# Performance work log

Measured on AMD Instinct MI355X. Metric: run time of the kernel, lower is better.

## Reference

```python
import jax, jax.numpy as jnp
import numpy as np

N_NODES = 50000
N_EDGES = 600000
D = 128        # input_dim == hidden_dim
OUT = 2        # output_dim
N_LAYERS = 6


def setup_inputs() -> dict:
    key = jax.random.key(0)
    ks = jax.random.split(key, 6)
    scale = 1.0 / np.sqrt(D)
    x = jax.random.normal(ks[0], (N_NODES, D), jnp.float32)
    edge_index = jax.random.randint(ks[1], (2, N_EDGES), 0, N_NODES)
    Wl = jax.random.normal(ks[2], (N_LAYERS, D, D), jnp.float32) * scale  # neighbor (lin_l) weights
    Wr = jax.random.normal(ks[3], (N_LAYERS, D, D), jnp.float32) * scale  # root (lin_r) weights
    bl = jnp.zeros((N_LAYERS, D), jnp.float32)                            # lin_l bias
    fc_W = jax.random.normal(ks[4], (D, OUT), jnp.float32) * scale
    fc_b = jnp.zeros((OUT,), jnp.float32)
    return {"x": x, "edge_index": edge_index, "Wl": Wl, "Wr": Wr, "bl": bl,
            "fc_W": fc_W, "fc_b": fc_b}


def _sage_conv(h, src, dst, deg_inv, Wl_i, Wr_i, bl_i):
    # mean aggregation over incoming edges: gather -> scatter-add -> normalize
    agg = jax.ops.segment_sum(h[src], dst, num_segments=h.shape[0]) * deg_inv  # [N, D]
    return agg @ Wl_i + h @ Wr_i + bl_i


def reference(x, edge_index, Wl, Wr, bl, fc_W, fc_b):
    src, dst = edge_index[0], edge_index[1]
    deg = jax.ops.segment_sum(jnp.ones(src.shape, x.dtype), dst, num_segments=x.shape[0])
    deg_inv = (1.0 / jnp.maximum(deg, 1.0))[:, None]  # [N, 1]
    h = x
    # ReLU follows every SAGEConv: inner act of each GraphSAGE block + explicit F.relu after each block
    for i in range(N_LAYERS):
        h = _sage_conv(h, src, dst, deg_inv, Wl[i], Wr[i], bl[i])
        h = jax.nn.relu(h)
    return h @ fc_W + fc_b  # [N, OUT]
```

## Files before the change

kernel.cpp:

```cpp
#include <hip/hip_runtime.h>
#include <hip/hip_bf16.h>

#define N_NODES 50000
#define N_EDGES 600000
#define DD 128
#define N_LAYERS 6
#define SCAN_BLOCKS 196
#define N_CHUNKS 3125
#define AGG_BLOCKS 6256

#define XB16_T 1600000
#define ZERO_T 50000
#define PREPW_T 196608
#define PREP_TOTAL (XB16_T + ZERO_T + PREPW_T)

typedef __attribute__((ext_vector_type(8))) short bf16x8;
typedef __attribute__((ext_vector_type(4))) float floatx4;

__device__ __forceinline__ void ldsdma16(const void* g, void* l) {
    __builtin_amdgcn_global_load_lds(
        (const __attribute__((address_space(1))) char*)g,
        (__attribute__((address_space(3))) char*)l, 16, 0, 0);
}

__device__ __forceinline__ unsigned short f2b(float f) {
    unsigned u = __float_as_uint(f);
    unsigned r = (u + 0x7FFFu + ((u >> 16) & 1u)) >> 16;
    return (unsigned short)r;
}


__global__ void prep_all(const float* __restrict__ x, unsigned short* __restrict__ hx,
                         const float* __restrict__ Wl, const float* __restrict__ Wr,
                         unsigned short* __restrict__ WT2,
                         int* __restrict__ deg, int* __restrict__ cursor) {
    int gid = blockIdx.x * blockDim.x + threadIdx.x;
    if (gid < XB16_T) {
        int b = gid * 4;
        float4 v = *(const float4*)(x + b);
        ushort4 o;
        o.x = f2b(v.x); o.y = f2b(v.y); o.z = f2b(v.z); o.w = f2b(v.w);
        *(ushort4*)(hx + b) = o;
    } else if (gid < XB16_T + ZERO_T) {
        int i = gid - XB16_T;
        deg[i] = 0; cursor[i] = 0;
    } else if (gid < PREP_TOTAL) {
        int idx = gid - (XB16_T + ZERO_T);
        int l   = idx >> 15;
        int rem = idx & 32767;
        int n   = rem >> 8;
        int k2  = rem & 255;
        const float* W = (k2 < 128 ? Wl : Wr) + (size_t)l * DD * DD + (size_t)(k2 & 127) * DD + n;
        WT2[idx] = f2b(*W);
    }
}


__global__ void count_deg(const int* __restrict__ dst, int* __restrict__ deg) {
    int e = blockIdx.x * blockDim.x + threadIdx.x;
    if (e < N_EDGES) atomicAdd(&deg[dst[e]], 1);
}

__global__ void block_sums(const int* __restrict__ deg, int* __restrict__ bsum) {
    __shared__ int s[256];
    int tid = threadIdx.x;
    int i = blockIdx.x * 256 + tid;
    int v = (i < N_NODES) ? deg[i] : 0;
    s[tid] = v;
    __syncthreads();
    #pragma unroll
    for (int off = 128; off > 0; off >>= 1) {
        if (tid < off) s[tid] += s[tid + off];
        __syncthreads();
    }
    if (tid == 0) bsum[blockIdx.x] = s[0];
}

__global__ void scan_bsums(int* __restrict__ bsum, int* __restrict__ offsets) {
    __shared__ int s[256];
    int tid = threadIdx.x;
    int v = (tid < SCAN_BLOCKS) ? bsum[tid] : 0;
    s[tid] = v;
    __syncthreads();
    for (int off = 1; off < 256; off <<= 1) {
        int t = (tid >= off) ? s[tid - off] : 0;
        __syncthreads();
        s[tid] += t;
        __syncthreads();
    }
    if (tid < SCAN_BLOCKS) bsum[tid] = s[tid] - v;
    if (tid == 0) offsets[N_NODES] = N_EDGES;
}

__global__ void write_offsets(const int* __restrict__ deg, const int* __restrict__ bsum,
                              int* __restrict__ offsets, float* __restrict__ deg_inv) {
    __shared__ int s[256];
    int tid = threadIdx.x;
    int i = blockIdx.x * 256 + tid;
    int v = (i < N_NODES) ? deg[i] : 0;
    s[tid] = v;
    __syncthreads();
    for (int off = 1; off < 256; off <<= 1) {
        int t = (tid >= off) ? s[tid - off] : 0;
        __syncthreads();
        s[tid] += t;
        __syncthreads();
    }
    if (i < N_NODES) {
        offsets[i] = bsum[blockIdx.x] + s[tid] - v;
        deg_inv[i] = 1.0f / (float)(v > 1 ? v : 1);
    }
}

__global__ void fill_csr(const int* __restrict__ src, const int* __restrict__ dst,
                         const int* __restrict__ offsets, int* __restrict__ cursor,
                         int* __restrict__ csr_src) {
    int e = blockIdx.x * blockDim.x + threadIdx.x;
    if (e < N_EDGES) {
        int d = dst[e];
        int p = atomicAdd(&cursor[d], 1);
        csr_src[offsets[d] + p] = src[e];
    }
}


__global__ void aggregate(const unsigned short* __restrict__ hin, const int* __restrict__ offsets,
                          const int* __restrict__ csr_src, const float* __restrict__ deg_inv,
                          unsigned short* __restrict__ agg) {
    int w    = threadIdx.x >> 6;
    int lane = threadIdx.x & 63;
    int nodeSel = lane >> 5;
    int l32  = lane & 31;
    int grp  = l32 >> 3;
    int p    = l32 & 7;

    int b = blockIdx.x;
    int x = b & 7, s = b >> 3;
    int hc = 16 * (s >> 1) + 2 * x + (s & 1);
    int node = hc * 8 + 2 * w + nodeSel;
    if (node >= N_NODES) return;
    int s0 = offsets[node], e0 = offsets[node + 1];
    float di = deg_inv[node];

    float a[16];
    #pragma unroll
    for (int i = 0; i < 16; ++i) a[i] = 0.f;

    const unsigned short* base = hin;
    int j = s0 + grp;
    for (; j + 4 < e0; j += 8) {
        int src1 = csr_src[j];
        int src2 = csr_src[j + 4];
        const uint4* r1 = (const uint4*)(base + (size_t)src1 * DD + p * 16);
        const uint4* r2 = (const uint4*)(base + (size_t)src2 * DD + p * 16);
        uint4 v1a = r1[0], v1b = r1[1];
        uint4 v2a = r2[0], v2b = r2[1];
        a[0] += __uint_as_float(v1a.x << 16); a[1] += __uint_as_float(v1a.x & 0xFFFF0000u);
        a[2] += __uint_as_float(v1a.y << 16); a[3] += __uint_as_float(v1a.y & 0xFFFF0000u);
        a[4] += __uint_as_float(v1a.z << 16); a[5] += __uint_as_float(v1a.z & 0xFFFF0000u);
        a[6] += __uint_as_float(v1a.w << 16); a[7] += __uint_as_float(v1a.w & 0xFFFF0000u);
        a[8] += __uint_as_float(v1b.x << 16); a[9] += __uint_as_float(v1b.x & 0xFFFF0000u);
        a[10]+= __uint_as_float(v1b.y << 16); a[11]+= __uint_as_float(v1b.y & 0xFFFF0000u);
        a[12]+= __uint_as_float(v1b.z << 16); a[13]+= __uint_as_float(v1b.z & 0xFFFF0000u);
        a[14]+= __uint_as_float(v1b.w << 16); a[15]+= __uint_as_float(v1b.w & 0xFFFF0000u);
        a[0] += __uint_as_float(v2a.x << 16); a[1] += __uint_as_float(v2a.x & 0xFFFF0000u);
        a[2] += __uint_as_float(v2a.y << 16); a[3] += __uint_as_float(v2a.y & 0xFFFF0000u);
        a[4] += __uint_as_float(v2a.z << 16); a[5] += __uint_as_float(v2a.z & 0xFFFF0000u);
        a[6] += __uint_as_float(v2a.w << 16); a[7] += __uint_as_float(v2a.w & 0xFFFF0000u);
        a[8] += __uint_as_float(v2b.x << 16); a[9] += __uint_as_float(v2b.x & 0xFFFF0000u);
        a[10]+= __uint_as_float(v2b.y << 16); a[11]+= __uint_as_float(v2b.y & 0xFFFF0000u);
        a[12]+= __uint_as_float(v2b.z << 16); a[13]+= __uint_as_float(v2b.z & 0xFFFF0000u);
        a[14]+= __uint_as_float(v2b.w << 16); a[15]+= __uint_as_float(v2b.w & 0xFFFF0000u);
    }
    if (j < e0) {
        int src1 = csr_src[j];
        const uint4* r1 = (const uint4*)(base + (size_t)src1 * DD + p * 16);
        uint4 v1a = r1[0], v1b = r1[1];
        a[0] += __uint_as_float(v1a.x << 16); a[1] += __uint_as_float(v1a.x & 0xFFFF0000u);
        a[2] += __uint_as_float(v1a.y << 16); a[3] += __uint_as_float(v1a.y & 0xFFFF0000u);
        a[4] += __uint_as_float(v1a.z << 16); a[5] += __uint_as_float(v1a.z & 0xFFFF0000u);
        a[6] += __uint_as_float(v1a.w << 16); a[7] += __uint_as_float(v1a.w & 0xFFFF0000u);
        a[8] += __uint_as_float(v1b.x << 16); a[9] += __uint_as_float(v1b.x & 0xFFFF0000u);
        a[10]+= __uint_as_float(v1b.y << 16); a[11]+= __uint_as_float(v1b.y & 0xFFFF0000u);
        a[12]+= __uint_as_float(v1b.z << 16); a[13]+= __uint_as_float(v1b.z & 0xFFFF0000u);
        a[14]+= __uint_as_float(v1b.w << 16); a[15]+= __uint_as_float(v1b.w & 0xFFFF0000u);
    }

    #pragma unroll
    for (int i = 0; i < 16; ++i) {
        a[i] += __shfl_xor(a[i], 8, 64);
        a[i] += __shfl_xor(a[i], 16, 64);
    }

    if (grp == 0) {
        uint4 o1, o2;
        o1.x = (unsigned)f2b(a[0] * di) | ((unsigned)f2b(a[1] * di) << 16);
        o1.y = (unsigned)f2b(a[2] * di) | ((unsigned)f2b(a[3] * di) << 16);
        o1.z = (unsigned)f2b(a[4] * di) | ((unsigned)f2b(a[5] * di) << 16);
        o1.w = (unsigned)f2b(a[6] * di) | ((unsigned)f2b(a[7] * di) << 16);
        o2.x = (unsigned)f2b(a[8] * di) | ((unsigned)f2b(a[9] * di) << 16);
        o2.y = (unsigned)f2b(a[10]* di) | ((unsigned)f2b(a[11]* di) << 16);
        o2.z = (unsigned)f2b(a[12]* di) | ((unsigned)f2b(a[13]* di) << 16);
        o2.w = (unsigned)f2b(a[14]* di) | ((unsigned)f2b(a[15]* di) << 16);
        uint4* dst = (uint4*)(agg + (size_t)node * DD + p * 16);
        dst[0] = o1;
        dst[1] = o2;
    }
}


__launch_bounds__(512, 2)
__global__ void gemm_resW(const unsigned short* __restrict__ Agg,
                          const unsigned short* __restrict__ H,
                          const unsigned short* __restrict__ WT2,
                          const float* __restrict__ bias,
                          unsigned short* __restrict__ Cout,
                          const float* __restrict__ fcW,
                          const float* __restrict__ fcb,
                          float* __restrict__ out,
                          int doFC) {
    __shared__ __align__(16) unsigned short sW[128 * 256];
    __shared__ __align__(16) unsigned short sA[8][4096];

    int tid  = threadIdx.x;
    int wid  = tid >> 6, lane = tid & 63;
    int l15  = lane & 15, q = lane >> 4;

    for (int t = tid; t < 4096; t += 512) {
        int col = t >> 5, c = t & 31;
        uint4 v = *(const uint4*)(WT2 + (size_t)col * 256 + c * 8);
        *(uint4*)(sW + ((size_t)col * 32 + (c ^ (col & 7))) * 8) = v;
    }
    __syncthreads();

    float bcol[8];
    #pragma unroll
    for (int j = 0; j < 8; ++j) bcol[j] = bias[j * 16 + l15];

    float2 fcw[8];
    float fb0 = 0.f, fb1 = 0.f;
    if (doFC) {
        #pragma unroll
        for (int j = 0; j < 8; ++j) fcw[j] = *(const float2*)(fcW + (j * 16 + l15) * 2);
        fb0 = fcb[0]; fb1 = fcb[1];
    }

    unsigned short* myA = &sA[wid][0];
    int x = blockIdx.x & 7, bb = blockIdx.x >> 3;

    for (int chunk = x + 8 * (bb * 8 + wid); chunk < N_CHUNKS; chunk += 2048) {
        int row0 = chunk * 16;
        #pragma unroll
        for (int i = 0; i < 4; ++i) {
            int r  = i * 4 + q;
            int cg = l15 ^ (r & 7);
            ldsdma16(Agg + (size_t)(row0 + r) * DD + cg * 8, myA + (size_t)i * 512 + lane * 8);
        }
        #pragma unroll
        for (int i = 0; i < 4; ++i) {
            int r  = i * 4 + q;
            int cg = l15 ^ (r & 7);
            ldsdma16(H + (size_t)(row0 + r) * DD + cg * 8, myA + 2048 + (size_t)i * 512 + lane * 8);
        }
        __builtin_amdgcn_s_waitcnt(0);

        floatx4 acc[8];
        #pragma unroll
        for (int j = 0; j < 8; ++j) acc[j] = (floatx4){0.f, 0.f, 0.f, 0.f};

        #pragma unroll
        for (int s = 0; s < 8; ++s) {
            int cglob = s * 4 + q;
            int reg   = cglob >> 4;
            int cin   = cglob & 15;
            bf16x8 aF = *(const bf16x8*)(myA + (size_t)reg * 2048 +
                                         ((size_t)l15 * 16 + (cin ^ (l15 & 7))) * 8);
            #pragma unroll
            for (int j = 0; j < 8; ++j) {
                int col = j * 16 + l15;
                bf16x8 bF = *(const bf16x8*)(sW + ((size_t)col * 32 + (cglob ^ (col & 7))) * 8);
                acc[j] = __builtin_amdgcn_mfma_f32_16x16x32_bf16(aF, bF, acc[j], 0, 0, 0);
            }
        }

        if (!doFC) {
            #pragma unroll
            for (int r = 0; r < 4; ++r) {
                int row = row0 + q * 4 + r;
                #pragma unroll
                for (int j = 0; j < 8; ++j) {
                    float v = acc[j][r] + bcol[j];
                    Cout[(size_t)row * DD + j * 16 + l15] = f2b(fmaxf(v, 0.f));
                }
            }
        } else {
            #pragma unroll
            for (int r = 0; r < 4; ++r) {
                float p0 = 0.f, p1 = 0.f;
                #pragma unroll
                for (int j = 0; j < 8; ++j) {
                    float v = fmaxf(acc[j][r] + bcol[j], 0.f);
                    p0 += v * fcw[j].x;
                    p1 += v * fcw[j].y;
                }
                p0 += __shfl_xor(p0, 1, 64); p1 += __shfl_xor(p1, 1, 64);
                p0 += __shfl_xor(p0, 2, 64); p1 += __shfl_xor(p1, 2, 64);
                p0 += __shfl_xor(p0, 4, 64); p1 += __shfl_xor(p1, 4, 64);
                p0 += __shfl_xor(p0, 8, 64); p1 += __shfl_xor(p1, 8, 64);
                if (l15 == 0) {
                    int row = row0 + q * 4 + r;
                    out[row * 2]     = p0 + fb0;
                    out[row * 2 + 1] = p1 + fb1;
                }
            }
        }
    }
}


extern "C" void kernel_launch(void* const* d_in, const int* in_sizes, int n_in,
                              void* d_out, int out_size, void* d_ws, size_t ws_size,
                              hipStream_t stream) {
    const float* x    = (const float*)d_in[0];
    const int*   ei   = (const int*)d_in[1];
    const float* Wl   = (const float*)d_in[2];
    const float* Wr   = (const float*)d_in[3];
    const float* bl   = (const float*)d_in[4];
    const float* fcW  = (const float*)d_in[5];
    const float* fcb  = (const float*)d_in[6];
    float* out = (float*)d_out;

    const int* srcIdx = ei;
    const int* dstIdx = ei + N_EDGES;

    char* ws = (char*)d_ws;
    size_t off = 0;
    auto bump = [&](size_t bytes) { char* p = ws + off; off = (off + bytes + 255) & ~(size_t)255; return p; };
    int*   deg     = (int*)  bump(N_NODES * 4);
    int*   cursor  = (int*)  bump(N_NODES * 4);
    int*   offsets = (int*)  bump((N_NODES + 1) * 4);
    int*   bsum    = (int*)  bump(SCAN_BLOCKS * 4);
    float* deg_inv = (float*)bump(N_NODES * 4);
    int*   csr     = (int*)  bump(N_EDGES * 4);
    unsigned short* hx   = (unsigned short*)bump((size_t)N_NODES * DD * 2);
    unsigned short* hb0  = (unsigned short*)bump((size_t)N_NODES * DD * 2);
    unsigned short* hb1  = (unsigned short*)bump((size_t)N_NODES * DD * 2);
    unsigned short* agg  = (unsigned short*)bump((size_t)N_NODES * DD * 2);
    unsigned short* WT2  = (unsigned short*)bump((size_t)N_LAYERS * 128 * 256 * 2);
    (void)ws_size;

    prep_all<<<(PREP_TOTAL + 255) / 256, 256, 0, stream>>>(x, hx, Wl, Wr, WT2, deg, cursor);
    count_deg<<<(N_EDGES + 255) / 256, 256, 0, stream>>>(dstIdx, deg);
    block_sums<<<SCAN_BLOCKS, 256, 0, stream>>>(deg, bsum);
    scan_bsums<<<1, 256, 0, stream>>>(bsum, offsets);
    write_offsets<<<SCAN_BLOCKS, 256, 0, stream>>>(deg, bsum, offsets, deg_inv);
    fill_csr<<<(N_EDGES + 255) / 256, 256, 0, stream>>>(srcIdx, dstIdx, offsets, cursor, csr);

    const unsigned short* hin = hx;
    unsigned short* hbuf[2] = { hb0, hb1 };
    for (int l = 0; l < N_LAYERS; ++l) {
        int last = (l == N_LAYERS - 1);
        aggregate<<<AGG_BLOCKS, 256, 0, stream>>>(hin, offsets, csr, deg_inv, agg);
        unsigned short* hout = hbuf[l & 1];
        gemm_resW<<<256, 512, 0, stream>>>(
            agg, hin, WT2 + (size_t)l * 128 * 256, bl + (size_t)l * DD, hout,
            fcW, fcb, out, last);
        hin = hout;
    }
}
```

Before: 347.4 us.

## Load GEMM A-fragments directly to registers and launch one chunk per wave

```diff
diff --git a/kernel.cpp b/kernel.cpp
--- a/kernel.cpp
+++ b/kernel.cpp
@@ -16,12 +16,6 @@
 
 typedef __attribute__((ext_vector_type(8))) short bf16x8;
 typedef __attribute__((ext_vector_type(4))) float floatx4;
-
-__device__ __forceinline__ void ldsdma16(const void* g, void* l) {
-    __builtin_amdgcn_global_load_lds(
-        (const __attribute__((address_space(1))) char*)g,
-        (__attribute__((address_space(3))) char*)l, 16, 0, 0);
-}
 
 __device__ __forceinline__ unsigned short f2b(float f) {
     unsigned u = __float_as_uint(f);
@@ -209,7 +203,7 @@
 }
 
 
-__launch_bounds__(512, 2)
+__launch_bounds__(512, 4)
 __global__ void gemm_resW(const unsigned short* __restrict__ Agg,
                           const unsigned short* __restrict__ H,
                           const unsigned short* __restrict__ WT2,
@@ -220,7 +214,6 @@
                           float* __restrict__ out,
                           int doFC) {
     __shared__ __align__(16) unsigned short sW[128 * 256];
-    __shared__ __align__(16) unsigned short sA[8][4096];
 
     int tid  = threadIdx.x;
     int wid  = tid >> 6, lane = tid & 63;
@@ -233,85 +226,71 @@
     }
     __syncthreads();
 
+    int chunk = blockIdx.x * 8 + wid;
+    if (chunk >= N_CHUNKS) return;
+    int row0 = chunk * 16;
+
     float bcol[8];
     #pragma unroll
     for (int j = 0; j < 8; ++j) bcol[j] = bias[j * 16 + l15];
 
-    float2 fcw[8];
-    float fb0 = 0.f, fb1 = 0.f;
-    if (doFC) {
+    const unsigned short* Arow = Agg + (size_t)(row0 + l15) * DD;
+    const unsigned short* Hrow = H   + (size_t)(row0 + l15) * DD;
+    bf16x8 aF[8];
+    #pragma unroll
+    for (int s = 0; s < 4; ++s)
+        aF[s] = *(const bf16x8*)(Arow + (s * 4 + q) * 8);
+    #pragma unroll
+    for (int s = 4; s < 8; ++s)
+        aF[s] = *(const bf16x8*)(Hrow + (s * 4 + q - 16) * 8);
+
+    floatx4 acc[8];
+    #pragma unroll
+    for (int j = 0; j < 8; ++j) acc[j] = (floatx4){0.f, 0.f, 0.f, 0.f};
+
+    #pragma unroll
+    for (int s = 0; s < 8; ++s) {
+        int cglob = s * 4 + q;
+        #pragma unroll
+        for (int j = 0; j < 8; ++j) {
+            int col = j * 16 + l15;
+            bf16x8 bF = *(const bf16x8*)(sW + ((size_t)col * 32 + (cglob ^ (col & 7))) * 8);
+            acc[j] = __builtin_amdgcn_mfma_f32_16x16x32_bf16(aF[s], bF, acc[j], 0, 0, 0);
+        }
+    }
+
+    if (!doFC) {
+        #pragma unroll
+        for (int r = 0; r < 4; ++r) {
+            int row = row0 + q * 4 + r;
+            #pragma unroll
+            for (int j = 0; j < 8; ++j) {
+                float v = acc[j][r] + bcol[j];
+                Cout[(size_t)row * DD + j * 16 + l15] = f2b(fmaxf(v, 0.f));
+            }
+        }
+    } else {
+        float2 fcw[8];
         #pragma unroll
         for (int j = 0; j < 8; ++j) fcw[j] = *(const float2*)(fcW + (j * 16 + l15) * 2);
-        fb0 = fcb[0]; fb1 = fcb[1];
-    }
-
-    unsigned short* myA = &sA[wid][0];
-    int x = blockIdx.x & 7, bb = blockIdx.x >> 3;
-
-    for (int chunk = x + 8 * (bb * 8 + wid); chunk < N_CHUNKS; chunk += 2048) {
-        int row0 = chunk * 16;
+        float fb0 = fcb[0], fb1 = fcb[1];
         #pragma unroll
-        for (int i = 0; i < 4; ++i) {
-            int r  = i * 4 + q;
-            int cg = l15 ^ (r & 7);
-            ldsdma16(Agg + (size_t)(row0 + r) * DD + cg * 8, myA + (size_t)i * 512 + lane * 8);
-        }
-        #pragma unroll
-        for (int i = 0; i < 4; ++i) {
-            int r  = i * 4 + q;
-            int cg = l15 ^ (r & 7);
-            ldsdma16(H + (size_t)(row0 + r) * DD + cg * 8, myA + 2048 + (size_t)i * 512 + lane * 8);
-        }
-        __builtin_amdgcn_s_waitcnt(0);
-
-        floatx4 acc[8];
-        #pragma unroll
-        for (int j = 0; j < 8; ++j) acc[j] = (floatx4){0.f, 0.f, 0.f, 0.f};
-
-        #pragma unroll
-        for (int s = 0; s < 8; ++s) {
-            int cglob = s * 4 + q;
-            int reg   = cglob >> 4;
-            int cin   = cglob & 15;
-            bf16x8 aF = *(const bf16x8*)(myA + (size_t)reg * 2048 +
-                                         ((size_t)l15 * 16 + (cin ^ (l15 & 7))) * 8);
+        for (int r = 0; r < 4; ++r) {
+            float p0 = 0.f, p1 = 0.f;
             #pragma unroll
             for (int j = 0; j < 8; ++j) {
-                int col = j * 16 + l15;
-                bf16x8 bF = *(const bf16x8*)(sW + ((size_t)col * 32 + (cglob ^ (col & 7))) * 8);
-                acc[j] = __builtin_amdgcn_mfma_f32_16x16x32_bf16(aF, bF, acc[j], 0, 0, 0);
+                float v = fmaxf(acc[j][r] + bcol[j], 0.f);
+                p0 += v * fcw[j].x;
+                p1 += v * fcw[j].y;
             }
-        }
-
-        if (!doFC) {
-            #pragma unroll
-            for (int r = 0; r < 4; ++r) {
+            p0 += __shfl_xor(p0, 1, 64); p1 += __shfl_xor(p1, 1, 64);
+            p0 += __shfl_xor(p0, 2, 64); p1 += __shfl_xor(p1, 2, 64);
+            p0 += __shfl_xor(p0, 4, 64); p1 += __shfl_xor(p1, 4, 64);
+            p0 += __shfl_xor(p0, 8, 64); p1 += __shfl_xor(p1, 8, 64);
+            if (l15 == 0) {
                 int row = row0 + q * 4 + r;
-                #pragma unroll
-                for (int j = 0; j < 8; ++j) {
-                    float v = acc[j][r] + bcol[j];
-                    Cout[(size_t)row * DD + j * 16 + l15] = f2b(fmaxf(v, 0.f));
-                }
-            }
-        } else {
-            #pragma unroll
-            for (int r = 0; r < 4; ++r) {
-                float p0 = 0.f, p1 = 0.f;
-                #pragma unroll
-                for (int j = 0; j < 8; ++j) {
-                    float v = fmaxf(acc[j][r] + bcol[j], 0.f);
-                    p0 += v * fcw[j].x;
-                    p1 += v * fcw[j].y;
-                }
-                p0 += __shfl_xor(p0, 1, 64); p1 += __shfl_xor(p1, 1, 64);
-                p0 += __shfl_xor(p0, 2, 64); p1 += __shfl_xor(p1, 2, 64);
-                p0 += __shfl_xor(p0, 4, 64); p1 += __shfl_xor(p1, 4, 64);
-                p0 += __shfl_xor(p0, 8, 64); p1 += __shfl_xor(p1, 8, 64);
-                if (l15 == 0) {
-                    int row = row0 + q * 4 + r;
-                    out[row * 2]     = p0 + fb0;
-                    out[row * 2 + 1] = p1 + fb1;
-                }
+                out[row * 2]     = p0 + fb0;
+                out[row * 2 + 1] = p1 + fb1;
             }
         }
     }
@@ -362,7 +341,7 @@
         int last = (l == N_LAYERS - 1);
         aggregate<<<AGG_BLOCKS, 256, 0, stream>>>(hin, offsets, csr, deg_inv, agg);
         unsigned short* hout = hbuf[l & 1];
-        gemm_resW<<<256, 512, 0, stream>>>(
+        gemm_resW<<<(N_CHUNKS + 7) / 8, 512, 0, stream>>>(
             agg, hin, WT2 + (size_t)l * 128 * 256, bl + (size_t)l * DD, hout,
             fcW, fcb, out, last);
         hin = hout;
```

Result: no change. 341.8 us (-1.6%).
